# Kernel tuning notes

Measured on AMD Instinct MI355X. Metric: run time of the kernel, lower is better.

The kernel has to match this reference:

```python
import jax, jax.numpy as jnp
import numpy as np

N = 50000   # nodes
E = 800000  # edges (avg degree 16)
D = 128     # in_features == out_features (residual)
NEG_SLOPE = 0.2
BN_EPS = 1e-5


def setup_inputs() -> dict:
    key = jax.random.key(0)
    ks = jax.random.split(key, 8)
    x = jax.random.normal(ks[0], (N, D), jnp.float32)
    edge_index = jax.random.randint(ks[1], (2, E), 0, N, dtype=jnp.int32)
    W = jax.random.normal(ks[2], (D, D), jnp.float32) * 0.05
    att_src = jax.random.normal(ks[3], (D,), jnp.float32) * 0.1
    att_dst = jax.random.normal(ks[4], (D,), jnp.float32) * 0.1
    bias = jax.random.normal(ks[5], (D,), jnp.float32) * 0.01
    gamma = jnp.ones((D,), jnp.float32) + jax.random.normal(ks[6], (D,), jnp.float32) * 0.05
    beta = jax.random.normal(ks[7], (D,), jnp.float32) * 0.05
    return {"x": x, "edge_index": edge_index, "W": W, "att_src": att_src,
            "att_dst": att_dst, "bias": bias, "gamma": gamma, "beta": beta}


def reference(x, edge_index, W, att_src, att_dst, bias, gamma, beta):
    src, dst = edge_index[0], edge_index[1]
    # Linear transform (GATConv lin)
    h = x @ W                                   # [N, D]
    # Per-node attention logit halves
    a_s = h @ att_src                           # [N]
    a_d = h @ att_dst                           # [N]
    # Per-edge logits + LeakyReLU
    e = jax.nn.leaky_relu(a_s[src] + a_d[dst], NEG_SLOPE)  # [E]
    # Segment softmax over destination neighborhoods
    m = jax.ops.segment_max(e, dst, num_segments=N)        # [N]
    m = jnp.where(jnp.isfinite(m), m, 0.0)
    p = jnp.exp(e - m[dst])                                 # [E]
    denom = jax.ops.segment_sum(p, dst, num_segments=N)    # [N]
    alpha = p / denom[dst]                                  # [E]
    # Scatter-aggregate weighted neighbor features
    y = jax.ops.segment_sum(alpha[:, None] * h[src], dst, num_segments=N)  # [N, D]
    y = y + bias
    # NormDropRes (eval mode): BN with running_mean=0, running_var=1; dropout off
    yn = gamma * (y / jnp.sqrt(1.0 + BN_EPS)) + beta
    yn = jax.nn.relu(yn)
    # residual: in==out so base = x
    return x + yn
```

## Files before the change

kernel.cpp:

```cpp
#include <hip/hip_runtime.h>
#include <math.h>

#define NN 50000
#define EE 800000
#define DD 128
#define NEG 0.2f
#define SLOT 48
#define NWIN 128
#define WIN 391
#define CAP 7168

typedef short bf16x8 __attribute__((ext_vector_type(8)));
typedef float f32x4  __attribute__((ext_vector_type(4)));
typedef int   i32x4  __attribute__((ext_vector_type(4)));

__device__ __forceinline__ unsigned short f2bf(float f) {
    unsigned u = __float_as_uint(f);
    unsigned r = u + 0x7fffu + ((u >> 16) & 1u);
    return (unsigned short)(r >> 16);
}

__global__ __launch_bounds__(256) void k_pre(
        const float* __restrict__ W, unsigned short* __restrict__ wt,
        int* __restrict__ win_cnt)
{
    const int t = threadIdx.x;
    if (blockIdx.x == 64) {
        if (t < NWIN) win_cnt[t] = 0;
        return;
    }
    int idx = blockIdx.x * 256 + t;
    int k = idx >> 7, n = idx & 127;
    wt[n * DD + k] = f2bf(W[idx]);
}

#define XS_STRIDE 136
__global__ __launch_bounds__(256) void k_A(
        const float* __restrict__ x, const unsigned short* __restrict__ wtg,
        const float* __restrict__ att_src, const float* __restrict__ att_dst,
        unsigned short* __restrict__ hb, float* __restrict__ a_s, float* __restrict__ a_d,
        const int* __restrict__ ei, int* __restrict__ win_cnt, unsigned* __restrict__ pairs)
{
    __shared__ __align__(16) short smem[26112];
    const int t = threadIdx.x;

    if (blockIdx.x & 1) {
        int* lcnt  = (int*)smem;
        int* lbase = (int*)smem + NWIN;
        if (t < NWIN) lcnt[t] = 0;
        __syncthreads();

        int idx = (int)(blockIdx.x >> 1) * 256 + t;
        int b[4], lp[4];
        unsigned v[4];
        bool valid = idx < EE / 4;
        if (valid) {
            i32x4 s4 = __builtin_nontemporal_load(&((const i32x4*)ei)[idx]);
            i32x4 d4 = __builtin_nontemporal_load(&((const i32x4*)(ei + EE))[idx]);
            b[0] = d4.x / WIN; v[0] = ((unsigned)(d4.x - b[0] * WIN) << 16) | (unsigned)s4.x;
            b[1] = d4.y / WIN; v[1] = ((unsigned)(d4.y - b[1] * WIN) << 16) | (unsigned)s4.y;
            b[2] = d4.z / WIN; v[2] = ((unsigned)(d4.z - b[2] * WIN) << 16) | (unsigned)s4.z;
            b[3] = d4.w / WIN; v[3] = ((unsigned)(d4.w - b[3] * WIN) << 16) | (unsigned)s4.w;
            lp[0] = atomicAdd(&lcnt[b[0]], 1);
            lp[1] = atomicAdd(&lcnt[b[1]], 1);
            lp[2] = atomicAdd(&lcnt[b[2]], 1);
            lp[3] = atomicAdd(&lcnt[b[3]], 1);
        }
        __syncthreads();
        if (t < NWIN) lbase[t] = atomicAdd(&win_cnt[t], lcnt[t]);
        __syncthreads();
        if (valid) {
#pragma unroll
            for (int k = 0; k < 4; k++) {
                int pos = lbase[b[k]] + lp[k];
                if (pos < CAP) pairs[(size_t)b[k] * CAP + pos] = v[k];
            }
        }
        return;
    }

    short* xs = smem;
    short* ws = smem + 64 * XS_STRIDE;
    const int row0 = (int)(blockIdx.x >> 1) * 64;

#pragma unroll
    for (int i = 0; i < 4; i++) {
        int idx = t + i * 256;
        int m = idx >> 4, c = idx & 15;
        int row = row0 + m;
        float4 f0 = make_float4(0.f, 0.f, 0.f, 0.f), f1 = f0;
        if (row < NN) {
            const float* p = x + (size_t)row * DD + c * 8;
            f0 = *(const float4*)p;
            f1 = *(const float4*)(p + 4);
        }
        bf16x8 v;
        v[0] = (short)f2bf(f0.x); v[1] = (short)f2bf(f0.y);
        v[2] = (short)f2bf(f0.z); v[3] = (short)f2bf(f0.w);
        v[4] = (short)f2bf(f1.x); v[5] = (short)f2bf(f1.y);
        v[6] = (short)f2bf(f1.z); v[7] = (short)f2bf(f1.w);
        *(bf16x8*)&xs[m * XS_STRIDE + c * 8] = v;
    }
#pragma unroll
    for (int i = 0; i < 8; i++) {
        int idx = t + i * 256;
        int n = idx >> 4, c = idx & 15;
        uint4 v = ((const uint4*)wtg)[idx];
        *(uint4*)&ws[n * XS_STRIDE + c * 8] = v;
    }
    __syncthreads();

    const int wv = t >> 6;
    const int lane = t & 63;
    const int n0 = lane & 15;
    const int quad = lane >> 4;

    bf16x8 afr[4];
#pragma unroll
    for (int kc = 0; kc < 4; kc++)
        afr[kc] = *(const bf16x8*)&xs[(wv * 16 + n0) * XS_STRIDE + kc * 32 + quad * 8];

    f32x4 acc[8];
#pragma unroll
    for (int nt = 0; nt < 8; nt++) {
        f32x4 a = {0.f, 0.f, 0.f, 0.f};
#pragma unroll
        for (int kc = 0; kc < 4; kc++) {
            bf16x8 bfr = *(const bf16x8*)&ws[(nt * 16 + n0) * XS_STRIDE + kc * 32 + quad * 8];
            a = __builtin_amdgcn_mfma_f32_16x16x32_bf16(afr[kc], bfr, a, 0, 0, 0);
        }
        acc[nt] = a;
    }

    const int rbase = row0 + wv * 16 + quad * 4;
    float ss[4] = {0.f, 0.f, 0.f, 0.f};
    float sd[4] = {0.f, 0.f, 0.f, 0.f};
#pragma unroll
    for (int nt = 0; nt < 8; nt++) {
        int col = nt * 16 + n0;
        float asc = att_src[col], adc = att_dst[col];
#pragma unroll
        for (int r = 0; r < 4; r++) {
            float v = acc[nt][r];
            ss[r] = fmaf(v, asc, ss[r]);
            sd[r] = fmaf(v, adc, sd[r]);
            int row = rbase + r;
            if (row < NN) hb[(size_t)row * DD + col] = f2bf(v);
        }
    }
#pragma unroll
    for (int r = 0; r < 4; r++) {
#pragma unroll
        for (int off = 1; off < 16; off <<= 1) {
            ss[r] += __shfl_xor(ss[r], off);
            sd[r] += __shfl_xor(sd[r], off);
        }
    }
    if (n0 == 0) {
#pragma unroll
        for (int r = 0; r < 4; r++) {
            int row = rbase + r;
            if (row < NN) { a_s[row] = ss[r]; a_d[row] = sd[r]; }
        }
    }
}

__global__ __launch_bounds__(512) void k_B(
        const int* __restrict__ win_cnt, const unsigned* __restrict__ pairs,
        int* __restrict__ cursor, unsigned short* __restrict__ slots)
{
    __shared__ int lcur[400];
    __shared__ __align__(16) unsigned short lslots[WIN * SLOT];
    const int t = threadIdx.x;
    const int w = blockIdx.x;

    for (int i = t; i < 400; i += 512) lcur[i] = 0;
    __syncthreads();

    int n = win_cnt[w]; if (n > CAP) n = CAP;
    const unsigned* pw = pairs + (size_t)w * CAP;
    for (int g = t; g < n; g += 512) {
        unsigned v = pw[g];
        int ld = (int)(v >> 16);
        int pos = atomicAdd(&lcur[ld], 1);
        if (pos < SLOT) lslots[ld * SLOT + pos] = (unsigned short)(v & 0xffffu);
    }
    __syncthreads();

    const uint4* src = (const uint4*)lslots;
    uint4* dst = (uint4*)(slots + (size_t)w * WIN * SLOT);
    for (int i = t; i < WIN * SLOT / 8; i += 512) dst[i] = src[i];
    int base = w * WIN;
    for (int i = t; i < WIN; i += 512) {
        int d = base + i;
        if (d < NN) cursor[d] = lcur[i];
    }
}

__global__ __launch_bounds__(256) void k_node(
        const int* __restrict__ cursor, const unsigned short* __restrict__ slots,
        const float* __restrict__ a_s, const float* __restrict__ a_d,
        const unsigned short* __restrict__ hb, const float* __restrict__ x,
        const float* __restrict__ bias, const float* __restrict__ gamma,
        const float* __restrict__ beta, float* __restrict__ out)
{
    int node = (int)((blockIdx.x * blockDim.x + threadIdx.x) >> 6);
    int lane = threadIdx.x & 63;
    if (node >= NN) return;

    int deg = cursor[node];
    deg = deg > SLOT ? SLOT : deg;
    float ad = a_d[node];

    int s = 0;
    float p = 0.f;
    if (lane < deg) {
        s = (int)slots[node * SLOT + lane];
        float e = a_s[s] + ad;
        e = e > 0.f ? e : NEG * e;
        p = __expf(e);
    }
    float l = p;
#pragma unroll
    for (int off = 32; off > 0; off >>= 1)
        l += __shfl_xor(l, off);

    const int eq = lane >> 4;
    const int fl = lane & 15;
    float acc[8];
#pragma unroll
    for (int k = 0; k < 8; k++) acc[k] = 0.f;

    for (int t = 0; t < deg; t += 8) {
        int i0 = t + eq, i1 = t + 4 + eq;
        int   st0 = __shfl(s, i0);
        int   st1 = __shfl(s, i1);
        float pt0 = __shfl(p, i0);
        float pt1 = __shfl(p, i1);
        uint4 hv0 = *(const uint4*)(hb + ((size_t)st0 << 7) + fl * 8);
        uint4 hv1 = *(const uint4*)(hb + ((size_t)st1 << 7) + fl * 8);
        acc[0] = fmaf(pt0, __uint_as_float(hv0.x << 16),          acc[0]);
        acc[1] = fmaf(pt0, __uint_as_float(hv0.x & 0xffff0000u),  acc[1]);
        acc[2] = fmaf(pt0, __uint_as_float(hv0.y << 16),          acc[2]);
        acc[3] = fmaf(pt0, __uint_as_float(hv0.y & 0xffff0000u),  acc[3]);
        acc[4] = fmaf(pt0, __uint_as_float(hv0.z << 16),          acc[4]);
        acc[5] = fmaf(pt0, __uint_as_float(hv0.z & 0xffff0000u),  acc[5]);
        acc[6] = fmaf(pt0, __uint_as_float(hv0.w << 16),          acc[6]);
        acc[7] = fmaf(pt0, __uint_as_float(hv0.w & 0xffff0000u),  acc[7]);
        acc[0] = fmaf(pt1, __uint_as_float(hv1.x << 16),          acc[0]);
        acc[1] = fmaf(pt1, __uint_as_float(hv1.x & 0xffff0000u),  acc[1]);
        acc[2] = fmaf(pt1, __uint_as_float(hv1.y << 16),          acc[2]);
        acc[3] = fmaf(pt1, __uint_as_float(hv1.y & 0xffff0000u),  acc[3]);
        acc[4] = fmaf(pt1, __uint_as_float(hv1.z << 16),          acc[4]);
        acc[5] = fmaf(pt1, __uint_as_float(hv1.z & 0xffff0000u),  acc[5]);
        acc[6] = fmaf(pt1, __uint_as_float(hv1.w << 16),          acc[6]);
        acc[7] = fmaf(pt1, __uint_as_float(hv1.w & 0xffff0000u),  acc[7]);
    }

#pragma unroll
    for (int off = 16; off < 64; off <<= 1) {
#pragma unroll
        for (int k = 0; k < 8; k++)
            acc[k] += __shfl_xor(acc[k], off);
    }

    if (eq == 0) {
        float invl = (deg > 0) ? 1.f / l : 0.f;
        const float invbn = 0.9999950000374997f;
        int c0 = fl * 8;
        const float* bp = bias  + c0;
        const float* gp = gamma + c0;
        const float* ep = beta  + c0;
        const float* xp = x + ((size_t)node << 7) + c0;
        float* op = out + ((size_t)node << 7) + c0;
        float4 o0, o1;
        float* oo[2] = {(float*)&o0, (float*)&o1};
#pragma unroll
        for (int k = 0; k < 8; k++) {
            float y  = acc[k] * invl + bp[k];
            float yn = gp[k] * (y * invbn) + ep[k];
            yn = yn > 0.f ? yn : 0.f;
            oo[k >> 2][k & 3] = xp[k] + yn;
        }
        *(float4*)op       = o0;
        *(float4*)(op + 4) = o1;
    }
}

extern "C" void kernel_launch(void* const* d_in, const int* in_sizes, int n_in,
                              void* d_out, int out_size, void* d_ws, size_t ws_size,
                              hipStream_t stream)
{
    const float* x     = (const float*)d_in[0];
    const int*   ei    = (const int*)  d_in[1];
    const float* W     = (const float*)d_in[2];
    const float* att_s = (const float*)d_in[3];
    const float* att_d = (const float*)d_in[4];
    const float* bias  = (const float*)d_in[5];
    const float* gamma = (const float*)d_in[6];
    const float* beta  = (const float*)d_in[7];
    float* out = (float*)d_out;

    int*            cursor  = (int*)d_ws;
    int*            win_cnt = cursor + NN;
    unsigned*       pairs   = (unsigned*)(win_cnt + NWIN);
    unsigned short* slots   = (unsigned short*)(pairs + (size_t)NWIN * CAP);
    float*          a_sv    = (float*)(slots + (size_t)NWIN * WIN * SLOT);
    float*          a_dv    = a_sv + NN;
    unsigned short* wtg     = (unsigned short*)(a_dv + NN);
    unsigned short* hb      = wtg + DD * DD;

    k_pre <<<65, 256, 0, stream>>>(W, wtg, win_cnt);
    k_A   <<<2 * ((NN + 63) / 64), 256, 0, stream>>>(x, wtg, att_s, att_d, hb,
                                                     a_sv, a_dv, ei, win_cnt, pairs);
    k_B   <<<NWIN, 512, 0, stream>>>(win_cnt, pairs, cursor, slots);
    k_node<<<(NN * 64 + 255) / 256, 256, 0, stream>>>(cursor, slots, a_sv, a_dv,
                                                       hb, x, bias, gamma, beta, out);
}
```

Baseline: 158.6 us.

## Fuse slot bucketing and per-node aggregation into one kernel using LDS slots

Merges the window bucketing kernel and the per-node softmax/aggregation kernel into a single kernel. Each window is split into four quarter-blocks, and each block keeps its local adjacency slots in shared memory and then processes those nodes directly. This removes the global slots/cursor round trip and one kernel launch. In exchange, each block rescans the whole window's pair list (four times the reads), and only 512 blocks of 8 waves each iterate over about 98 nodes, which reduces parallelism compared with one wave per node.

```diff
diff --git a/kernel.cpp b/kernel.cpp
--- a/kernel.cpp
+++ b/kernel.cpp
@@ -9,6 +9,7 @@
 #define NWIN 128
 #define WIN 391
 #define CAP 7168
+#define QW 98
 
 typedef short bf16x8 __attribute__((ext_vector_type(8)));
 typedef float f32x4  __attribute__((ext_vector_type(4)));
@@ -165,16 +166,23 @@
     }
 }
 
-__global__ __launch_bounds__(512) void k_B(
+__global__ __launch_bounds__(512) void k_BN(
         const int* __restrict__ win_cnt, const unsigned* __restrict__ pairs,
-        int* __restrict__ cursor, unsigned short* __restrict__ slots)
+        const float* __restrict__ a_s, const float* __restrict__ a_d,
+        const unsigned short* __restrict__ hb, const float* __restrict__ x,
+        const float* __restrict__ bias, const float* __restrict__ gamma,
+        const float* __restrict__ beta, float* __restrict__ out)
 {
-    __shared__ int lcur[400];
-    __shared__ __align__(16) unsigned short lslots[WIN * SLOT];
+    __shared__ int lcur[QW];
+    __shared__ __align__(16) unsigned short lslots[QW * SLOT];
     const int t = threadIdx.x;
-    const int w = blockIdx.x;
-
-    for (int i = t; i < 400; i += 512) lcur[i] = 0;
+    const int w = (int)(blockIdx.x >> 2);
+    const int q = (int)(blockIdx.x & 3);
+    const int lo = q * QW;
+    int hi = lo + QW; if (hi > WIN) hi = WIN;
+    const int nloc = hi - lo;
+
+    for (int i = t; i < QW; i += 512) lcur[i] = 0;
     __syncthreads();
 
     int n = win_cnt[w]; if (n > CAP) n = CAP;
@@ -182,108 +190,97 @@
     for (int g = t; g < n; g += 512) {
         unsigned v = pw[g];
         int ld = (int)(v >> 16);
-        int pos = atomicAdd(&lcur[ld], 1);
-        if (pos < SLOT) lslots[ld * SLOT + pos] = (unsigned short)(v & 0xffffu);
+        if (ld >= lo && ld < hi) {
+            int pos = atomicAdd(&lcur[ld - lo], 1);
+            if (pos < SLOT) lslots[(ld - lo) * SLOT + pos] = (unsigned short)(v & 0xffffu);
+        }
     }
     __syncthreads();
 
-    const uint4* src = (const uint4*)lslots;
-    uint4* dst = (uint4*)(slots + (size_t)w * WIN * SLOT);
-    for (int i = t; i < WIN * SLOT / 8; i += 512) dst[i] = src[i];
-    int base = w * WIN;
-    for (int i = t; i < WIN; i += 512) {
-        int d = base + i;
-        if (d < NN) cursor[d] = lcur[i];
-    }
-}
-
-__global__ __launch_bounds__(256) void k_node(
-        const int* __restrict__ cursor, const unsigned short* __restrict__ slots,
-        const float* __restrict__ a_s, const float* __restrict__ a_d,
-        const unsigned short* __restrict__ hb, const float* __restrict__ x,
-        const float* __restrict__ bias, const float* __restrict__ gamma,
-        const float* __restrict__ beta, float* __restrict__ out)
-{
-    int node = (int)((blockIdx.x * blockDim.x + threadIdx.x) >> 6);
-    int lane = threadIdx.x & 63;
-    if (node >= NN) return;
-
-    int deg = cursor[node];
-    deg = deg > SLOT ? SLOT : deg;
-    float ad = a_d[node];
-
-    int s = 0;
-    float p = 0.f;
-    if (lane < deg) {
-        s = (int)slots[node * SLOT + lane];
-        float e = a_s[s] + ad;
-        e = e > 0.f ? e : NEG * e;
-        p = __expf(e);
-    }
-    float l = p;
-#pragma unroll
-    for (int off = 32; off > 0; off >>= 1)
-        l += __shfl_xor(l, off);
-
+    const int wv = t >> 6;
+    const int lane = t & 63;
     const int eq = lane >> 4;
     const int fl = lane & 15;
-    float acc[8];
-#pragma unroll
-    for (int k = 0; k < 8; k++) acc[k] = 0.f;
-
-    for (int t = 0; t < deg; t += 8) {
-        int i0 = t + eq, i1 = t + 4 + eq;
-        int   st0 = __shfl(s, i0);
-        int   st1 = __shfl(s, i1);
-        float pt0 = __shfl(p, i0);
-        float pt1 = __shfl(p, i1);
-        uint4 hv0 = *(const uint4*)(hb + ((size_t)st0 << 7) + fl * 8);
-        uint4 hv1 = *(const uint4*)(hb + ((size_t)st1 << 7) + fl * 8);
-        acc[0] = fmaf(pt0, __uint_as_float(hv0.x << 16),          acc[0]);
-        acc[1] = fmaf(pt0, __uint_as_float(hv0.x & 0xffff0000u),  acc[1]);
-        acc[2] = fmaf(pt0, __uint_as_float(hv0.y << 16),          acc[2]);
-        acc[3] = fmaf(pt0, __uint_as_float(hv0.y & 0xffff0000u),  acc[3]);
-        acc[4] = fmaf(pt0, __uint_as_float(hv0.z << 16),          acc[4]);
-        acc[5] = fmaf(pt0, __uint_as_float(hv0.z & 0xffff0000u),  acc[5]);
-        acc[6] = fmaf(pt0, __uint_as_float(hv0.w << 16),          acc[6]);
-        acc[7] = fmaf(pt0, __uint_as_float(hv0.w & 0xffff0000u),  acc[7]);
-        acc[0] = fmaf(pt1, __uint_as_float(hv1.x << 16),          acc[0]);
-        acc[1] = fmaf(pt1, __uint_as_float(hv1.x & 0xffff0000u),  acc[1]);
-        acc[2] = fmaf(pt1, __uint_as_float(hv1.y << 16),          acc[2]);
-        acc[3] = fmaf(pt1, __uint_as_float(hv1.y & 0xffff0000u),  acc[3]);
-        acc[4] = fmaf(pt1, __uint_as_float(hv1.z << 16),          acc[4]);
-        acc[5] = fmaf(pt1, __uint_as_float(hv1.z & 0xffff0000u),  acc[5]);
-        acc[6] = fmaf(pt1, __uint_as_float(hv1.w << 16),          acc[6]);
-        acc[7] = fmaf(pt1, __uint_as_float(hv1.w & 0xffff0000u),  acc[7]);
-    }
-
-#pragma unroll
-    for (int off = 16; off < 64; off <<= 1) {
-#pragma unroll
-        for (int k = 0; k < 8; k++)
-            acc[k] += __shfl_xor(acc[k], off);
-    }
-
-    if (eq == 0) {
-        float invl = (deg > 0) ? 1.f / l : 0.f;
-        const float invbn = 0.9999950000374997f;
-        int c0 = fl * 8;
-        const float* bp = bias  + c0;
-        const float* gp = gamma + c0;
-        const float* ep = beta  + c0;
-        const float* xp = x + ((size_t)node << 7) + c0;
-        float* op = out + ((size_t)node << 7) + c0;
-        float4 o0, o1;
-        float* oo[2] = {(float*)&o0, (float*)&o1};
-#pragma unroll
-        for (int k = 0; k < 8; k++) {
-            float y  = acc[k] * invl + bp[k];
-            float yn = gp[k] * (y * invbn) + ep[k];
-            yn = yn > 0.f ? yn : 0.f;
-            oo[k >> 2][k & 3] = xp[k] + yn;
-        }
-        *(float4*)op       = o0;
-        *(float4*)(op + 4) = o1;
+    const float invbn = 0.9999950000374997f;
+
+    for (int nl = wv; nl < nloc; nl += 8) {
+        int node = w * WIN + lo + nl;
+        if (node >= NN) break;
+
+        int deg = lcur[nl];
+        deg = deg > SLOT ? SLOT : deg;
+        float ad = a_d[node];
+
+        int s = 0;
+        float p = 0.f;
+        if (lane < deg) {
+            s = (int)lslots[nl * SLOT + lane];
+            float e = a_s[s] + ad;
+            e = e > 0.f ? e : NEG * e;
+            p = __expf(e);
+        }
+        float l = p;
+#pragma unroll
+        for (int off = 32; off > 0; off >>= 1)
+            l += __shfl_xor(l, off);
+
+        float acc[8];
+#pragma unroll
+        for (int k = 0; k < 8; k++) acc[k] = 0.f;
+
+        for (int tt = 0; tt < deg; tt += 8) {
+            int i0 = tt + eq, i1 = tt + 4 + eq;
+            int   st0 = __shfl(s, i0);
+            int   st1 = __shfl(s, i1);
+            float pt0 = __shfl(p, i0);
+            float pt1 = __shfl(p, i1);
+            uint4 hv0 = *(const uint4*)(hb + ((size_t)st0 << 7) + fl * 8);
+            uint4 hv1 = *(const uint4*)(hb + ((size_t)st1 << 7) + fl * 8);
+            acc[0] = fmaf(pt0, __uint_as_float(hv0.x << 16),          acc[0]);
+            acc[1] = fmaf(pt0, __uint_as_float(hv0.x & 0xffff0000u),  acc[1]);
+            acc[2] = fmaf(pt0, __uint_as_float(hv0.y << 16),          acc[2]);
+            acc[3] = fmaf(pt0, __uint_as_float(hv0.y & 0xffff0000u),  acc[3]);
+            acc[4] = fmaf(pt0, __uint_as_float(hv0.z << 16),          acc[4]);
+            acc[5] = fmaf(pt0, __uint_as_float(hv0.z & 0xffff0000u),  acc[5]);
+            acc[6] = fmaf(pt0, __uint_as_float(hv0.w << 16),          acc[6]);
+            acc[7] = fmaf(pt0, __uint_as_float(hv0.w & 0xffff0000u),  acc[7]);
+            acc[0] = fmaf(pt1, __uint_as_float(hv1.x << 16),          acc[0]);
+            acc[1] = fmaf(pt1, __uint_as_float(hv1.x & 0xffff0000u),  acc[1]);
+            acc[2] = fmaf(pt1, __uint_as_float(hv1.y << 16),          acc[2]);
+            acc[3] = fmaf(pt1, __uint_as_float(hv1.y & 0xffff0000u),  acc[3]);
+            acc[4] = fmaf(pt1, __uint_as_float(hv1.z << 16),          acc[4]);
+            acc[5] = fmaf(pt1, __uint_as_float(hv1.z & 0xffff0000u),  acc[5]);
+            acc[6] = fmaf(pt1, __uint_as_float(hv1.w << 16),          acc[6]);
+            acc[7] = fmaf(pt1, __uint_as_float(hv1.w & 0xffff0000u),  acc[7]);
+        }
+
+#pragma unroll
+        for (int off = 16; off < 64; off <<= 1) {
+#pragma unroll
+            for (int k = 0; k < 8; k++)
+                acc[k] += __shfl_xor(acc[k], off);
+        }
+
+        if (eq == 0) {
+            float invl = (deg > 0) ? 1.f / l : 0.f;
+            int c0 = fl * 8;
+            const float* bp = bias  + c0;
+            const float* gp = gamma + c0;
+            const float* ep = beta  + c0;
+            const float* xp = x + ((size_t)node << 7) + c0;
+            float* op = out + ((size_t)node << 7) + c0;
+            float4 o0, o1;
+            float* oo[2] = {(float*)&o0, (float*)&o1};
+#pragma unroll
+            for (int k = 0; k < 8; k++) {
+                float y  = acc[k] * invl + bp[k];
+                float yn = gp[k] * (y * invbn) + ep[k];
+                yn = yn > 0.f ? yn : 0.f;
+                oo[k >> 2][k & 3] = xp[k] + yn;
+            }
+            *(float4*)op       = o0;
+            *(float4*)(op + 4) = o1;
+        }
     }
 }
 
@@ -301,11 +298,9 @@
     const float* beta  = (const float*)d_in[7];
     float* out = (float*)d_out;
 
-    int*            cursor  = (int*)d_ws;
-    int*            win_cnt = cursor + NN;
+    int*            win_cnt = (int*)d_ws;
     unsigned*       pairs   = (unsigned*)(win_cnt + NWIN);
-    unsigned short* slots   = (unsigned short*)(pairs + (size_t)NWIN * CAP);
-    float*          a_sv    = (float*)(slots + (size_t)NWIN * WIN * SLOT);
+    float*          a_sv    = (float*)(pairs + (size_t)NWIN * CAP);
     float*          a_dv    = a_sv + NN;
     unsigned short* wtg     = (unsigned short*)(a_dv + NN);
     unsigned short* hb      = wtg + DD * DD;
@@ -313,7 +308,6 @@
     k_pre <<<65, 256, 0, stream>>>(W, wtg, win_cnt);
     k_A   <<<2 * ((NN + 63) / 64), 256, 0, stream>>>(x, wtg, att_s, att_d, hb,
                                                      a_sv, a_dv, ei, win_cnt, pairs);
-    k_B   <<<NWIN, 512, 0, stream>>>(win_cnt, pairs, cursor, slots);
-    k_node<<<(NN * 64 + 255) / 256, 256, 0, stream>>>(cursor, slots, a_sv, a_dv,
-                                                       hb, x, bias, gamma, beta, out);
-}
+    k_BN  <<<4 * NWIN, 512, 0, stream>>>(win_cnt, pairs, a_sv, a_dv,
+                                         hb, x, bias, gamma, beta, out);
+}
```

Result: faster. 154.0 us (-2.9%).
